# Kernel optimization log

Hardware: AMD Instinct MI355X
Metric: run time of the kernel (lower is better)

The kernel has to match this reference:

```python
import jax, jax.numpy as jnp
import numpy as np


def setup_inputs() -> dict:
    key = jax.random.key(0)
    ks = jax.random.split(key, 8)
    B, S, F, K, E, N = 20000, 10, 128, 16, 128, 200000
    nodes = jax.random.randint(ks[0], (B,), 0, N)
    neigh_idx = jax.random.randint(ks[1], (B, S), 0, N)
    self_table = jax.random.normal(ks[2], (N, F), dtype=jnp.float32)
    neigh_table = jax.random.normal(ks[3], (N, F), dtype=jnp.float32)
    center = jax.random.normal(ks[4], (K, F), dtype=jnp.float32)
    cluster_mask = jax.random.uniform(ks[5], (K, F), dtype=jnp.float32)
    # xavier-like scaling keeps exp(relu(.)) in a sane range
    weight = jax.random.normal(ks[6], (E, 2 * F), dtype=jnp.float32) * 0.05
    alpha = jax.random.normal(ks[7], (2 * F, 1), dtype=jnp.float32) * 0.05
    return {"nodes": nodes, "neigh_idx": neigh_idx, "self_table": self_table,
            "neigh_table": neigh_table, "center": center, "cluster_mask": cluster_mask,
            "weight": weight, "alpha": alpha}


def reference(nodes, neigh_idx, self_table, neigh_table, center, cluster_mask, weight, alpha):
    B, S = neigh_idx.shape
    F = self_table.shape[1]
    self_feat = self_table[nodes]                       # (B, F)
    neigh = neigh_table[neigh_idx]                      # (B, S, F) gather (== mask.matmul in original)
    # attention over sampled neighbors: exp(relu([self || neigh] @ alpha))
    a_self, a_neigh = alpha[:F, 0], alpha[F:, 0]        # split cat-matmul
    logits = self_feat @ a_self                         # (B,)
    logits = logits[:, None] + neigh @ a_neigh          # (B, S)
    att = jnp.exp(jax.nn.relu(logits))
    att_norm = att / jnp.sum(att, axis=1, keepdims=True)
    # inverse-distance soft assignment to k centers (Student-t, degree 1)
    n2 = jnp.sum(neigh * neigh, axis=-1)                # (B, S)
    c2 = jnp.sum(center * center, axis=-1)              # (K,)
    cross = jnp.einsum('bsf,kf->bsk', neigh, center)    # (B, S, K)
    q = 1.0 / (n2[:, :, None] - 2.0 * cross + c2[None, None, :] + 1.0)  # (B, S, K)
    # clustered features: sum_k q[b,s,k] * mask[k,f] * neigh[b,s,f]
    clustered = neigh * jnp.einsum('bsk,kf->bsf', q, cluster_mask)      # (B, S, F)
    neigh_agg = jnp.sum(clustered * att_norm[:, :, None], axis=1)       # (B, F)
    combined = jnp.concatenate([self_feat, neigh_agg], axis=1)          # (B, 2F)
    return jax.nn.relu(combined @ weight.T)                             # (B, E)
```

## Files before the change

### kernel.cpp

```cpp
#include <hip/hip_runtime.h>
#include <hip/hip_bf16.h>

typedef unsigned short ushort_t;
typedef __attribute__((ext_vector_type(4))) float v4f;
typedef __attribute__((ext_vector_type(8))) short v8s;

#define FDIM 128
#define KCLUST 16
#define CSTRIDE 264

__device__ __forceinline__ ushort_t f2bf(float x) {
    unsigned int u = __float_as_uint(x);
    unsigned int r = (u + 0x7fffu + ((u >> 16) & 1u)) >> 16;
    return (ushort_t)r;
}

__device__ __forceinline__ float wave_reduce_sum(float v) {
    #pragma unroll
    for (int off = 32; off > 0; off >>= 1) v += __shfl_xor(v, off, 64);
    return v;
}

__global__ void pack_weight(const float* __restrict__ W, ushort_t* __restrict__ Wb,
                            long total, long valid) {
    long i = ((long)blockIdx.x * blockDim.x + threadIdx.x) * 4;
    if (i >= total) return;
    float4 v;
    if (i < valid) v = *(const float4*)(W + i);
    else           v = make_float4(0.f, 0.f, 0.f, 0.f);
    ushort_t* dst = Wb + i;
    dst[0] = f2bf(v.x); dst[1] = f2bf(v.y); dst[2] = f2bf(v.z); dst[3] = f2bf(v.w);
}

__global__ __launch_bounds__(256) void fused_agg(
    const int* __restrict__ nodes, const int* __restrict__ neigh_idx,
    const float* __restrict__ self_table, const float* __restrict__ neigh_table,
    const float* __restrict__ center, const float* __restrict__ cluster_mask,
    const float* __restrict__ alpha, const ushort_t* __restrict__ Wb,
    float* __restrict__ out, int B, int S, int E) {

    __shared__ __align__(16) ushort_t comb[16 * CSTRIDE];
    __shared__ __align__(16) float nbuf[4 * 144];
    __shared__ __align__(16) float qbuf[4 * 16];

    int t = threadIdx.x;
    int lane = t & 63, wave = t >> 6;
    int kcl = lane & 15, blk = lane >> 4;
    int l16 = lane & 15, quad = lane >> 4;

    float as0 = alpha[lane],       as1 = alpha[lane + 64];
    float an0 = alpha[128 + lane], an1 = alpha[192 + lane];

    float cc[32];
    {
        const float* cb = center + kcl * FDIM + blk * 32;
        #pragma unroll
        for (int j = 0; j < 32; j += 4) {
            float4 v = *(const float4*)(cb + j);
            cc[j] = v.x; cc[j+1] = v.y; cc[j+2] = v.z; cc[j+3] = v.w;
        }
    }
    float mk0[KCLUST], mk1[KCLUST];
    #pragma unroll
    for (int kk = 0; kk < KCLUST; kk++) {
        mk0[kk] = cluster_mask[kk * FDIM + lane];
        mk1[kk] = cluster_mask[kk * FDIM + 64 + lane];
    }

    int b0 = blockIdx.x * 16;
    float* nb = nbuf + wave * 144;
    float* qb = qbuf + wave * 16;

    for (int r = 0; r < 4; r++) {
        int row = wave * 4 + r;
        int b = b0 + row;
        ushort_t* crow = comb + row * CSTRIDE;
        if (b >= B) {
            crow[lane] = 0; crow[lane + 64] = 0;
            crow[lane + 128] = 0; crow[lane + 192] = 0;
            continue;
        }
        size_t node = (size_t)nodes[b];
        float s0 = self_table[node * FDIM + lane];
        float s1 = self_table[node * FDIM + 64 + lane];
        float logit_self = wave_reduce_sum(s0 * as0 + s1 * as1);

        float acc0 = 0.f, acc1 = 0.f, attsum = 0.f;
        size_t g = (size_t)neigh_idx[(size_t)b * S];
        float n0 = neigh_table[g * FDIM + lane];
        float n1 = neigh_table[g * FDIM + 64 + lane];
        for (int s = 0; s < S; s++) {
            float cn0 = n0, cn1 = n1;
            if (s + 1 < S) {
                g = (size_t)neigh_idx[(size_t)b * S + s + 1];
                n0 = neigh_table[g * FDIM + lane];
                n1 = neigh_table[g * FDIM + 64 + lane];
            }
            float ln = wave_reduce_sum(cn0 * an0 + cn1 * an1);
            float att = __expf(fmaxf(logit_self + ln, 0.f));
            nb[lane + (lane >> 5) * 4] = cn0;
            int f2 = lane + 64;
            nb[f2 + (f2 >> 5) * 4] = cn1;
            float d = 0.f;
            const float* nbb = nb + blk * 36;
            #pragma unroll
            for (int i = 0; i < 8; i++) {
                float4 f4 = *(const float4*)(nbb + i * 4);
                float t0 = f4.x - cc[i*4+0]; d = fmaf(t0, t0, d);
                float t1 = f4.y - cc[i*4+1]; d = fmaf(t1, t1, d);
                float t2 = f4.z - cc[i*4+2]; d = fmaf(t2, t2, d);
                float t3 = f4.w - cc[i*4+3]; d = fmaf(t3, t3, d);
            }
            d += __shfl_xor(d, 16, 64);
            d += __shfl_xor(d, 32, 64);
            float q = 1.0f / (d + 1.0f);
            if (lane < 16) qb[lane] = q;
            float4 q0 = *(const float4*)(qb + 0);
            float4 q1 = *(const float4*)(qb + 4);
            float4 q2 = *(const float4*)(qb + 8);
            float4 q3 = *(const float4*)(qb + 12);
            float m0, m1;
            m0  = q0.x*mk0[0]  + q0.y*mk0[1]  + q0.z*mk0[2]  + q0.w*mk0[3];
            m0 += q1.x*mk0[4]  + q1.y*mk0[5]  + q1.z*mk0[6]  + q1.w*mk0[7];
            m0 += q2.x*mk0[8]  + q2.y*mk0[9]  + q2.z*mk0[10] + q2.w*mk0[11];
            m0 += q3.x*mk0[12] + q3.y*mk0[13] + q3.z*mk0[14] + q3.w*mk0[15];
            m1  = q0.x*mk1[0]  + q0.y*mk1[1]  + q0.z*mk1[2]  + q0.w*mk1[3];
            m1 += q1.x*mk1[4]  + q1.y*mk1[5]  + q1.z*mk1[6]  + q1.w*mk1[7];
            m1 += q2.x*mk1[8]  + q2.y*mk1[9]  + q2.z*mk1[10] + q2.w*mk1[11];
            m1 += q3.x*mk1[12] + q3.y*mk1[13] + q3.z*mk1[14] + q3.w*mk1[15];
            acc0 += att * cn0 * m0;
            acc1 += att * cn1 * m1;
            attsum += att;
        }
        float inv = 1.0f / attsum;
        crow[lane]       = f2bf(s0);
        crow[lane + 64]  = f2bf(s1);
        crow[lane + 128] = f2bf(acc0 * inv);
        crow[lane + 192] = f2bf(acc1 * inv);
    }
    __syncthreads();

    v8s afr[8];
    #pragma unroll
    for (int kk = 0; kk < 8; kk++)
        afr[kk] = *(const v8s*)(comb + l16 * CSTRIDE + kk * 32 + quad * 8);

    int Ntiles = (E + 15) >> 4;
    for (int nt = wave; nt < Ntiles; nt += 4) {
        const ushort_t* wrow = Wb + ((size_t)(nt * 16 + l16)) * 256 + quad * 8;
        v4f acc = {0.f, 0.f, 0.f, 0.f};
        #pragma unroll
        for (int kk = 0; kk < 8; kk++) {
            v8s bfr = *(const v8s*)(wrow + kk * 32);
            acc = __builtin_amdgcn_mfma_f32_16x16x32_bf16(afr[kk], bfr, acc, 0, 0, 0);
        }
        int gcol = nt * 16 + l16;
        if (gcol < E) {
            #pragma unroll
            for (int rr = 0; rr < 4; rr++) {
                int grow = b0 + quad * 4 + rr;
                if (grow < B)
                    out[(size_t)grow * E + gcol] = fmaxf(acc[rr], 0.f);
            }
        }
    }
}

extern "C" void kernel_launch(void* const* d_in, const int* in_sizes, int n_in,
                              void* d_out, int out_size, void* d_ws, size_t ws_size,
                              hipStream_t stream) {
    const int*   nodes        = (const int*)d_in[0];
    const int*   neigh_idx    = (const int*)d_in[1];
    const float* self_table   = (const float*)d_in[2];
    const float* neigh_table  = (const float*)d_in[3];
    const float* center       = (const float*)d_in[4];
    const float* cluster_mask = (const float*)d_in[5];
    const float* weight       = (const float*)d_in[6];
    const float* alpha        = (const float*)d_in[7];
    float* out = (float*)d_out;

    int B = in_sizes[0];
    int S = in_sizes[1] / B;
    int E = in_sizes[6] / (2 * FDIM);

    int Np = ((E + 15) / 16) * 16;
    ushort_t* Wb = (ushort_t*)d_ws;

    long totalW = (long)Np * 256;
    long validW = (long)E * 256;
    int blksW = (int)((totalW + 1023) / 1024);
    pack_weight<<<blksW, 256, 0, stream>>>(weight, Wb, totalW, validW);

    int nblk = (B + 15) / 16;
    fused_agg<<<nblk, 256, 0, stream>>>(
        nodes, neigh_idx, self_table, neigh_table, center, cluster_mask, alpha,
        Wb, out, B, S, E);
}
```

Measured before the change: 279.9 us.

## Assign one batch row per wave with 512-thread blocks and fuse attention logit

```diff
diff --git a/kernel.cpp b/kernel.cpp
--- a/kernel.cpp
+++ b/kernel.cpp
@@ -32,7 +32,7 @@
     dst[0] = f2bf(v.x); dst[1] = f2bf(v.y); dst[2] = f2bf(v.z); dst[3] = f2bf(v.w);
 }
 
-__global__ __launch_bounds__(256) void fused_agg(
+__global__ __launch_bounds__(512, 6) void fused_agg(
     const int* __restrict__ nodes, const int* __restrict__ neigh_idx,
     const float* __restrict__ self_table, const float* __restrict__ neigh_table,
     const float* __restrict__ center, const float* __restrict__ cluster_mask,
@@ -40,24 +40,34 @@
     float* __restrict__ out, int B, int S, int E) {
 
     __shared__ __align__(16) ushort_t comb[16 * CSTRIDE];
-    __shared__ __align__(16) float nbuf[4 * 144];
-    __shared__ __align__(16) float qbuf[4 * 16];
+    __shared__ __align__(16) float nbuf[8 * 144];
+    __shared__ __align__(16) float qbuf[8 * 16];
 
     int t = threadIdx.x;
     int lane = t & 63, wave = t >> 6;
-    int kcl = lane & 15, blk = lane >> 4;
     int l16 = lane & 15, quad = lane >> 4;
 
-    float as0 = alpha[lane],       as1 = alpha[lane + 64];
-    float an0 = alpha[128 + lane], an1 = alpha[192 + lane];
+    for (int i = t; i < (8 * CSTRIDE) / 2; i += 512)
+        ((unsigned*)(comb + 8 * CSTRIDE))[i] = 0u;
+
+    float as0 = alpha[lane], as1 = alpha[lane + 64];
 
     float cc[32];
     {
-        const float* cb = center + kcl * FDIM + blk * 32;
+        const float* cb = center + l16 * FDIM + quad * 32;
         #pragma unroll
         for (int j = 0; j < 32; j += 4) {
             float4 v = *(const float4*)(cb + j);
             cc[j] = v.x; cc[j+1] = v.y; cc[j+2] = v.z; cc[j+3] = v.w;
+        }
+    }
+    float anc[32];
+    {
+        const float* ab = alpha + 128 + quad * 32;
+        #pragma unroll
+        for (int j = 0; j < 32; j += 4) {
+            float4 v = *(const float4*)(ab + j);
+            anc[j] = v.x; anc[j+1] = v.y; anc[j+2] = v.z; anc[j+3] = v.w;
         }
     }
     float mk0[KCLUST], mk1[KCLUST];
@@ -67,53 +77,47 @@
         mk1[kk] = cluster_mask[kk * FDIM + 64 + lane];
     }
 
-    int b0 = blockIdx.x * 16;
+    int b0 = blockIdx.x * 8;
+    int b = b0 + wave;
     float* nb = nbuf + wave * 144;
     float* qb = qbuf + wave * 16;
-
-    for (int r = 0; r < 4; r++) {
-        int row = wave * 4 + r;
-        int b = b0 + row;
-        ushort_t* crow = comb + row * CSTRIDE;
-        if (b >= B) {
-            crow[lane] = 0; crow[lane + 64] = 0;
-            crow[lane + 128] = 0; crow[lane + 192] = 0;
-            continue;
-        }
+    ushort_t* crow = comb + wave * CSTRIDE;
+
+    if (b < B) {
         size_t node = (size_t)nodes[b];
         float s0 = self_table[node * FDIM + lane];
         float s1 = self_table[node * FDIM + 64 + lane];
-        float logit_self = wave_reduce_sum(s0 * as0 + s1 * as1);
+        float ls = wave_reduce_sum(s0 * as0 + s1 * as1);
 
         float acc0 = 0.f, acc1 = 0.f, attsum = 0.f;
-        size_t g = (size_t)neigh_idx[(size_t)b * S];
+        const int* nidx = neigh_idx + (size_t)b * S;
+        size_t g = (size_t)nidx[0];
         float n0 = neigh_table[g * FDIM + lane];
         float n1 = neigh_table[g * FDIM + 64 + lane];
         for (int s = 0; s < S; s++) {
             float cn0 = n0, cn1 = n1;
             if (s + 1 < S) {
-                g = (size_t)neigh_idx[(size_t)b * S + s + 1];
+                g = (size_t)nidx[s + 1];
                 n0 = neigh_table[g * FDIM + lane];
                 n1 = neigh_table[g * FDIM + 64 + lane];
             }
-            float ln = wave_reduce_sum(cn0 * an0 + cn1 * an1);
-            float att = __expf(fmaxf(logit_self + ln, 0.f));
             nb[lane + (lane >> 5) * 4] = cn0;
             int f2 = lane + 64;
             nb[f2 + (f2 >> 5) * 4] = cn1;
-            float d = 0.f;
-            const float* nbb = nb + blk * 36;
+            float d = 0.f, lnp = 0.f;
+            const float* nbb = nb + quad * 36;
             #pragma unroll
             for (int i = 0; i < 8; i++) {
                 float4 f4 = *(const float4*)(nbb + i * 4);
-                float t0 = f4.x - cc[i*4+0]; d = fmaf(t0, t0, d);
-                float t1 = f4.y - cc[i*4+1]; d = fmaf(t1, t1, d);
-                float t2 = f4.z - cc[i*4+2]; d = fmaf(t2, t2, d);
-                float t3 = f4.w - cc[i*4+3]; d = fmaf(t3, t3, d);
+                float t0 = f4.x - cc[i*4+0]; d = fmaf(t0, t0, d); lnp = fmaf(f4.x, anc[i*4+0], lnp);
+                float t1 = f4.y - cc[i*4+1]; d = fmaf(t1, t1, d); lnp = fmaf(f4.y, anc[i*4+1], lnp);
+                float t2 = f4.z - cc[i*4+2]; d = fmaf(t2, t2, d); lnp = fmaf(f4.z, anc[i*4+2], lnp);
+                float t3 = f4.w - cc[i*4+3]; d = fmaf(t3, t3, d); lnp = fmaf(f4.w, anc[i*4+3], lnp);
             }
-            d += __shfl_xor(d, 16, 64);
-            d += __shfl_xor(d, 32, 64);
-            float q = 1.0f / (d + 1.0f);
+            d   += __shfl_xor(d, 16, 64);   d   += __shfl_xor(d, 32, 64);
+            lnp += __shfl_xor(lnp, 16, 64); lnp += __shfl_xor(lnp, 32, 64);
+            float att = __expf(fmaxf(ls + lnp, 0.f));
+            float q = __fdividef(att, d + 1.0f);
             if (lane < 16) qb[lane] = q;
             float4 q0 = *(const float4*)(qb + 0);
             float4 q1 = *(const float4*)(qb + 4);
@@ -128,15 +132,18 @@
             m1 += q1.x*mk1[4]  + q1.y*mk1[5]  + q1.z*mk1[6]  + q1.w*mk1[7];
             m1 += q2.x*mk1[8]  + q2.y*mk1[9]  + q2.z*mk1[10] + q2.w*mk1[11];
             m1 += q3.x*mk1[12] + q3.y*mk1[13] + q3.z*mk1[14] + q3.w*mk1[15];
-            acc0 += att * cn0 * m0;
-            acc1 += att * cn1 * m1;
+            acc0 += cn0 * m0;
+            acc1 += cn1 * m1;
             attsum += att;
         }
-        float inv = 1.0f / attsum;
+        float inv = __fdividef(1.0f, attsum);
         crow[lane]       = f2bf(s0);
         crow[lane + 64]  = f2bf(s1);
         crow[lane + 128] = f2bf(acc0 * inv);
         crow[lane + 192] = f2bf(acc1 * inv);
+    } else {
+        crow[lane] = 0; crow[lane + 64] = 0;
+        crow[lane + 128] = 0; crow[lane + 192] = 0;
     }
     __syncthreads();
 
@@ -146,7 +153,7 @@
         afr[kk] = *(const v8s*)(comb + l16 * CSTRIDE + kk * 32 + quad * 8);
 
     int Ntiles = (E + 15) >> 4;
-    for (int nt = wave; nt < Ntiles; nt += 4) {
+    for (int nt = wave; nt < Ntiles; nt += 8) {
         const ushort_t* wrow = Wb + ((size_t)(nt * 16 + l16)) * 256 + quad * 8;
         v4f acc = {0.f, 0.f, 0.f, 0.f};
         #pragma unroll
@@ -158,9 +165,12 @@
         if (gcol < E) {
             #pragma unroll
             for (int rr = 0; rr < 4; rr++) {
-                int grow = b0 + quad * 4 + rr;
-                if (grow < B)
-                    out[(size_t)grow * E + gcol] = fmaxf(acc[rr], 0.f);
+                int r16 = quad * 4 + rr;
+                if (r16 < 8) {
+                    int grow = b0 + r16;
+                    if (grow < B)
+                        out[(size_t)grow * E + gcol] = fmaxf(acc[rr], 0.f);
+                }
             }
         }
     }
@@ -191,8 +201,8 @@
     int blksW = (int)((totalW + 1023) / 1024);
     pack_weight<<<blksW, 256, 0, stream>>>(weight, Wb, totalW, validW);
 
-    int nblk = (B + 15) / 16;
-    fused_agg<<<nblk, 256, 0, stream>>>(
+    int nblk = (B + 7) / 8;
+    fused_agg<<<nblk, 512, 0, stream>>>(
         nodes, neigh_idx, self_table, neigh_table, center, cluster_mask, alpha,
         Wb, out, B, S, E);
 }
```

Result: slower. 779.1 us (+178.4%).

## Assign one batch row per wave and quadruple grid size

Applied to the files above, without the earlier changes.

```diff
diff --git a/kernel.cpp b/kernel.cpp
--- a/kernel.cpp
+++ b/kernel.cpp
@@ -45,15 +45,17 @@
 
     int t = threadIdx.x;
     int lane = t & 63, wave = t >> 6;
-    int kcl = lane & 15, blk = lane >> 4;
     int l16 = lane & 15, quad = lane >> 4;
+
+    for (int i = t; i < (12 * CSTRIDE) / 2; i += 256)
+        ((unsigned*)(comb + 4 * CSTRIDE))[i] = 0u;
 
     float as0 = alpha[lane],       as1 = alpha[lane + 64];
     float an0 = alpha[128 + lane], an1 = alpha[192 + lane];
 
     float cc[32];
     {
-        const float* cb = center + kcl * FDIM + blk * 32;
+        const float* cb = center + l16 * FDIM + quad * 32;
         #pragma unroll
         for (int j = 0; j < 32; j += 4) {
             float4 v = *(const float4*)(cb + j);
@@ -67,42 +69,37 @@
         mk1[kk] = cluster_mask[kk * FDIM + 64 + lane];
     }
 
-    int b0 = blockIdx.x * 16;
+    int b0 = blockIdx.x * 4;
+    int b = b0 + wave;
     float* nb = nbuf + wave * 144;
     float* qb = qbuf + wave * 16;
-
-    for (int r = 0; r < 4; r++) {
-        int row = wave * 4 + r;
-        int b = b0 + row;
-        ushort_t* crow = comb + row * CSTRIDE;
-        if (b >= B) {
-            crow[lane] = 0; crow[lane + 64] = 0;
-            crow[lane + 128] = 0; crow[lane + 192] = 0;
-            continue;
-        }
+    ushort_t* crow = comb + wave * CSTRIDE;
+
+    if (b < B) {
         size_t node = (size_t)nodes[b];
         float s0 = self_table[node * FDIM + lane];
         float s1 = self_table[node * FDIM + 64 + lane];
-        float logit_self = wave_reduce_sum(s0 * as0 + s1 * as1);
+        float ls = wave_reduce_sum(s0 * as0 + s1 * as1);
 
         float acc0 = 0.f, acc1 = 0.f, attsum = 0.f;
-        size_t g = (size_t)neigh_idx[(size_t)b * S];
+        const int* nidx = neigh_idx + (size_t)b * S;
+        size_t g = (size_t)nidx[0];
         float n0 = neigh_table[g * FDIM + lane];
         float n1 = neigh_table[g * FDIM + 64 + lane];
         for (int s = 0; s < S; s++) {
             float cn0 = n0, cn1 = n1;
             if (s + 1 < S) {
-                g = (size_t)neigh_idx[(size_t)b * S + s + 1];
+                g = (size_t)nidx[s + 1];
                 n0 = neigh_table[g * FDIM + lane];
                 n1 = neigh_table[g * FDIM + 64 + lane];
             }
             float ln = wave_reduce_sum(cn0 * an0 + cn1 * an1);
-            float att = __expf(fmaxf(logit_self + ln, 0.f));
+            float att = __expf(fmaxf(ls + ln, 0.f));
             nb[lane + (lane >> 5) * 4] = cn0;
             int f2 = lane + 64;
             nb[f2 + (f2 >> 5) * 4] = cn1;
             float d = 0.f;
-            const float* nbb = nb + blk * 36;
+            const float* nbb = nb + quad * 36;
             #pragma unroll
             for (int i = 0; i < 8; i++) {
                 float4 f4 = *(const float4*)(nbb + i * 4);
@@ -113,7 +110,7 @@
             }
             d += __shfl_xor(d, 16, 64);
             d += __shfl_xor(d, 32, 64);
-            float q = 1.0f / (d + 1.0f);
+            float q = __fdividef(att, d + 1.0f);
             if (lane < 16) qb[lane] = q;
             float4 q0 = *(const float4*)(qb + 0);
             float4 q1 = *(const float4*)(qb + 4);
@@ -128,15 +125,18 @@
             m1 += q1.x*mk1[4]  + q1.y*mk1[5]  + q1.z*mk1[6]  + q1.w*mk1[7];
             m1 += q2.x*mk1[8]  + q2.y*mk1[9]  + q2.z*mk1[10] + q2.w*mk1[11];
             m1 += q3.x*mk1[12] + q3.y*mk1[13] + q3.z*mk1[14] + q3.w*mk1[15];
-            acc0 += att * cn0 * m0;
-            acc1 += att * cn1 * m1;
+            acc0 += cn0 * m0;
+            acc1 += cn1 * m1;
             attsum += att;
         }
-        float inv = 1.0f / attsum;
+        float inv = __fdividef(1.0f, attsum);
         crow[lane]       = f2bf(s0);
         crow[lane + 64]  = f2bf(s1);
         crow[lane + 128] = f2bf(acc0 * inv);
         crow[lane + 192] = f2bf(acc1 * inv);
+    } else {
+        crow[lane] = 0; crow[lane + 64] = 0;
+        crow[lane + 128] = 0; crow[lane + 192] = 0;
     }
     __syncthreads();
 
@@ -158,9 +158,12 @@
         if (gcol < E) {
             #pragma unroll
             for (int rr = 0; rr < 4; rr++) {
-                int grow = b0 + quad * 4 + rr;
-                if (grow < B)
-                    out[(size_t)grow * E + gcol] = fmaxf(acc[rr], 0.f);
+                int r16 = quad * 4 + rr;
+                if (r16 < 4) {
+                    int grow = b0 + r16;
+                    if (grow < B)
+                        out[(size_t)grow * E + gcol] = fmaxf(acc[rr], 0.f);
+                }
             }
         }
     }
@@ -191,7 +194,7 @@
     int blksW = (int)((totalW + 1023) / 1024);
     pack_weight<<<blksW, 256, 0, stream>>>(weight, Wb, totalW, validW);
 
-    int nblk = (B + 15) / 16;
+    int nblk = (B + 3) / 4;
     fused_agg<<<nblk, 256, 0, stream>>>(
         nodes, neigh_idx, self_table, neigh_table, center, cluster_mask, alpha,
         Wb, out, B, S, E);
```

Measured after the change: 285.2 us. Within noise of the previous version (+1.9%).
